# Optimization experiments

Measured on AMD Instinct MI355X. Metric: run time of the kernel, lower is better.

The kernel has to match this reference:

```python
import jax, jax.numpy as jnp
import numpy as np

N = 8192
NUM_CLASSES = 81            # background + 80 fg classes (COCO)
SCORE_THRESH = 0.05
NMS_THRESH = 0.5
NUM_DETECTIONS = 100
REG_W = (10.0, 10.0, 5.0, 5.0)
MIN_SIZE = 1.0
BBOX_XFORM_CLIP = float(np.log(1000.0 / 16.0))


def setup_inputs() -> dict:
    key = jax.random.key(0)
    k1, k2, k3, k4 = jax.random.split(key, 4)
    xy1 = jax.random.uniform(k1, (N, 2), minval=0.0, maxval=700.0)
    wh = jax.random.uniform(k2, (N, 2), minval=8.0, maxval=300.0)
    proposal = jnp.concatenate([xy1, xy1 + wh], axis=1)          # [N,4] xyxy
    class_logit = jax.random.normal(k3, (N, NUM_CLASSES), dtype=jnp.float32)
    box_regression = jax.random.normal(k4, (N, NUM_CLASSES * 4), dtype=jnp.float32) * 0.5
    return {"proposal": proposal, "class_logit": class_logit,
            "box_regression": box_regression, "image_h": 800, "image_w": 1216}


def _decode(deltas, boxes):
    # deltas [..., N, 4] (per-class), boxes [N, 4] xyxy; standard Fast R-CNN BoxCoder.decode
    wx, wy, ww, wh = REG_W
    widths = boxes[:, 2] - boxes[:, 0]
    heights = boxes[:, 3] - boxes[:, 1]
    cx = boxes[:, 0] + 0.5 * widths
    cy = boxes[:, 1] + 0.5 * heights
    dx = deltas[..., 0] / wx
    dy = deltas[..., 1] / wy
    dw = jnp.minimum(deltas[..., 2] / ww, BBOX_XFORM_CLIP)
    dh = jnp.minimum(deltas[..., 3] / wh, BBOX_XFORM_CLIP)
    pcx = dx * widths + cx
    pcy = dy * heights + cy
    pw = jnp.exp(dw) * widths
    ph = jnp.exp(dh) * heights
    return jnp.stack([pcx - 0.5 * pw, pcy - 0.5 * ph,
                      pcx + 0.5 * pw, pcy + 0.5 * ph], axis=-1)


def _iou_one(box, boxes):
    # IoU of one box [4] against all boxes [N,4]
    lt = jnp.maximum(box[:2], boxes[:, :2])
    rb = jnp.minimum(box[2:], boxes[:, 2:])
    whc = jnp.clip(rb - lt, 0.0)
    inter = whc[:, 0] * whc[:, 1]
    a1 = (box[2] - box[0]) * (box[3] - box[1])
    a2 = (boxes[:, 2] - boxes[:, 0]) * (boxes[:, 3] - boxes[:, 1])
    return inter / (a1 + a2 - inter + 1e-12)


def _nms_per_class(boxes, scores):
    # Sequential greedy NMS: pick highest score, suppress IoU>thresh, repeat.
    # boxes [N,4], scores [N] (already 0 where filtered). Returns top NUM_DETECTIONS.
    def step(scores_w, _):
        j = jnp.argmax(scores_w)
        s = scores_w[j]
        valid = s > 0.0
        bj = boxes[j]
        iou = _iou_one(bj, boxes)                         # [N]
        new = jnp.where(iou > NMS_THRESH, 0.0, scores_w).at[j].set(0.0)
        new = jnp.where(valid, new, scores_w)
        return new, (bj, s, valid)
    _, (sel_b, sel_s, sel_v) = jax.lax.scan(step, scores, None, length=NUM_DETECTIONS)
    return sel_b, sel_s, sel_v                            # [D,4], [D], [D]


def reference(proposal, class_logit, box_regression, image_h, image_w):
    pred_score = jax.nn.softmax(class_logit, axis=-1)     # [N, C]
    deltas = box_regression.reshape(N, NUM_CLASSES, 4)
    fg_deltas = jnp.transpose(deltas[:, 1:, :], (1, 0, 2))  # [C-1, N, 4]
    boxes = _decode(fg_deltas, proposal)                    # [C-1, N, 4]
    # clip to image (process_box)
    W = jnp.float32(image_w); H = jnp.float32(image_h)
    x1 = jnp.clip(boxes[..., 0], 0.0, W)
    y1 = jnp.clip(boxes[..., 1], 0.0, H)
    x2 = jnp.clip(boxes[..., 2], 0.0, W)
    y2 = jnp.clip(boxes[..., 3], 0.0, H)
    boxes = jnp.stack([x1, y1, x2, y2], axis=-1)            # [C-1, N, 4]
    keep_size = ((x2 - x1) >= MIN_SIZE) & ((y2 - y1) >= MIN_SIZE)
    scores = jnp.transpose(pred_score[:, 1:])               # [C-1, N]
    scores = jnp.where((scores >= SCORE_THRESH) & keep_size, scores, 0.0)
    sel_b, sel_s, sel_v = jax.vmap(_nms_per_class)(boxes, scores)  # [C-1,D,...]
    out_boxes = sel_b.reshape(-1, 4)                         # [(C-1)*D, 4]
    out_scores = sel_s.reshape(-1)
    out_labels = jnp.repeat(jnp.arange(1, NUM_CLASSES, dtype=jnp.int32), NUM_DETECTIONS)
    out_valid = sel_v.reshape(-1)
    return out_boxes, out_scores, out_labels, out_valid
```

## Files before the change

kernel.cpp:

```cpp
#include <hip/hip_runtime.h>
#include <hip/hip_bf16.h>

#define NN 8192
#define NC 81
#define FG 80
#define ND 100
#define SH 8
#define CAPS 128
#define CPADI 32
#define MAXK 384
#define KW6 6
#define KROW 8
#define BBOX_CLIP 4.135166556742356f

__global__ __launch_bounds__(256) void decode_kernel(
    const float* __restrict__ prop,
    const float* __restrict__ logit,
    const float* __restrict__ reg,
    const int* __restrict__ ih, const int* __restrict__ iw,
    int* __restrict__ counts,
    float* __restrict__ boxes0,
    float* __restrict__ cbox,
    float* __restrict__ cscore)
{
    const int n = blockIdx.x * 4 + (threadIdx.x >> 6);
    const int shard = blockIdx.x & (SH - 1);
    const int lane = threadIdx.x & 63;
    const float* lrow = logit + (long)n * NC;

    float v1 = lrow[lane];
    float v2 = (lane < NC - 64) ? lrow[64 + lane] : -1e30f;
    float m = fmaxf(v1, v2);
#pragma unroll
    for (int off = 32; off; off >>= 1) m = fmaxf(m, __shfl_xor(m, off));
    float e = expf(v1 - m) + ((lane < NC - 64) ? expf(v2 - m) : 0.0f);
#pragma unroll
    for (int off = 32; off; off >>= 1) e += __shfl_xor(e, off);

    const float W = (float)iw[0];
    const float H = (float)ih[0];
    const float4 p = *(const float4*)(prop + n * 4);
    const float pw = p.z - p.x, ph = p.w - p.y;
    const float pcx = p.x + 0.5f * pw, pcy = p.y + 0.5f * ph;

    for (int c = 1 + lane; c <= FG; c += 64) {
        float score = expf(lrow[c] - m) / e;
        const float4 d = *(const float4*)(reg + (long)n * (NC * 4) + c * 4);
        float dx = d.x / 10.0f;
        float dy = d.y / 10.0f;
        float dw = fminf(d.z / 5.0f, BBOX_CLIP);
        float dh = fminf(d.w / 5.0f, BBOX_CLIP);
        float ncx = dx * pw + pcx;
        float ncy = dy * ph + pcy;
        float nw = expf(dw) * pw;
        float nh = expf(dh) * ph;
        float bx1 = ncx - 0.5f * nw, by1 = ncy - 0.5f * nh;
        float bx2 = ncx + 0.5f * nw, by2 = ncy + 0.5f * nh;
        bx1 = fminf(fmaxf(bx1, 0.0f), W);
        by1 = fminf(fmaxf(by1, 0.0f), H);
        bx2 = fminf(fmaxf(bx2, 0.0f), W);
        by2 = fminf(fmaxf(by2, 0.0f), H);
        bool keep = ((bx2 - bx1) >= 1.0f) && ((by2 - by1) >= 1.0f);

        if (n == 0) {
            float* b0 = boxes0 + (c - 1) * 4;
            b0[0] = bx1; b0[1] = by1; b0[2] = bx2; b0[3] = by2;
        }
        if (score >= 0.05f && keep) {
            const int slot = (c - 1) * SH + shard;
            int pos = atomicAdd(&counts[slot * CPADI], 1);
            if (pos < CAPS) {
                float* cb = cbox + ((long)slot * CAPS + pos) * 4;
                cb[0] = bx1; cb[1] = by1; cb[2] = bx2; cb[3] = by2;
                cscore[slot * CAPS + pos] = score;
            }
        }
    }
}

__global__ __launch_bounds__(1024) void nms_kernel(
    const int* __restrict__ counts,
    const float* __restrict__ boxes0,
    const float* __restrict__ cbox,
    const float* __restrict__ cscore,
    float* __restrict__ out)
{
    __shared__ __align__(16) float  s_sc[MAXK];
    __shared__ float4 s_ubox[MAXK];
    __shared__ int    s_sidx[MAXK];
    __shared__ float4 s_box[MAXK];
    __shared__ float  s_ss[MAXK];
    __shared__ unsigned long long s_row[MAXK * KROW];

    const int c = blockIdx.x;
    const int t = threadIdx.x;
    const int lane = t & 63;
    const int wv = t >> 6;

    int cnt0 = min(counts[(c * SH + 0) * CPADI], CAPS);
    int cnt1 = min(counts[(c * SH + 1) * CPADI], CAPS);
    int cnt2 = min(counts[(c * SH + 2) * CPADI], CAPS);
    int cnt3 = min(counts[(c * SH + 3) * CPADI], CAPS);
    int cnt4 = min(counts[(c * SH + 4) * CPADI], CAPS);
    int cnt5 = min(counts[(c * SH + 5) * CPADI], CAPS);
    int cnt6 = min(counts[(c * SH + 6) * CPADI], CAPS);
    int cnt7 = min(counts[(c * SH + 7) * CPADI], CAPS);
    int K = cnt0 + cnt1 + cnt2 + cnt3 + cnt4 + cnt5 + cnt6 + cnt7;
    if (K > MAXK) K = MAXK;
    const int KW = (K + 63) >> 6;

    for (int i = t; i < MAXK * KROW; i += 1024) s_row[i] = 0ull;
    for (int i = K + t; i < MAXK; i += 1024) {
        s_sc[i] = 0.0f;
        s_ss[i] = 0.0f;
        s_box[i] = make_float4(0.f, 0.f, 0.f, 0.f);
    }
    {
        const int s = t >> 7;
        const int i = t & (CAPS - 1);
        int mycnt = cnt0;
        if (s == 1) mycnt = cnt1; if (s == 2) mycnt = cnt2;
        if (s == 3) mycnt = cnt3; if (s == 4) mycnt = cnt4;
        if (s == 5) mycnt = cnt5; if (s == 6) mycnt = cnt6;
        if (s == 7) mycnt = cnt7;
        int offs = 0;
        if (s > 0) offs += cnt0; if (s > 1) offs += cnt1;
        if (s > 2) offs += cnt2; if (s > 3) offs += cnt3;
        if (s > 4) offs += cnt4; if (s > 5) offs += cnt5;
        if (s > 6) offs += cnt6;
        if (i < mycnt) {
            int d = offs + i;
            if (d < MAXK) {
                const long src = (long)(c * SH + s) * CAPS + i;
                s_sc[d] = cscore[src];
                s_ubox[d] = *(const float4*)(cbox + src * 4);
            }
        }
    }
    __syncthreads();

    if (t < K) {
        const float si = s_sc[t];
        const float4* s4 = (const float4*)s_sc;
        const int nch = (K + 3) >> 2;
        int r = 0;
        for (int ch = 0; ch < nch; ++ch) {
            const float4 sj = s4[ch];
            const int j = ch * 4;
            r += (sj.x > si) || (sj.x == si && (j + 0) < t);
            r += (sj.y > si) || (sj.y == si && (j + 1) < t);
            r += (sj.z > si) || (sj.z == si && (j + 2) < t);
            r += (sj.w > si) || (sj.w == si && (j + 3) < t);
        }
        s_sidx[r] = t;
    }
    __syncthreads();

    if (t < K) {
        const int i = s_sidx[t];
        s_box[t] = s_ubox[i];
        s_ss[t] = s_sc[i];
    }
    __syncthreads();

    float4 colb[KW6];
    float a2c[KW6];
#pragma unroll
    for (int w = 0; w < KW6; ++w) {
        const float4 b = s_box[w * 64 + lane];
        colb[w] = b;
        a2c[w] = (b.z - b.x) * (b.w - b.y);
    }

    for (int r = wv; r < K; r += 16) {
        const float4 rb = s_box[r];
        const float a1 = (rb.z - rb.x) * (rb.w - rb.y);
        const int w0 = r >> 6;
#pragma unroll
        for (int w = 0; w < KW6; ++w) {
            if (w >= w0 && w < KW) {
                const int j = w * 64 + lane;
                const float lx = fmaxf(rb.x, colb[w].x);
                const float ly = fmaxf(rb.y, colb[w].y);
                const float rx = fminf(rb.z, colb[w].z);
                const float ry = fminf(rb.w, colb[w].w);
                const float cw = fmaxf(rx - lx, 0.0f);
                const float ch = fmaxf(ry - ly, 0.0f);
                const float inter = cw * ch;
                const float iou = inter / (a1 + a2c[w] - inter + 1e-12f);
                const bool sup = (iou > 0.5f) && (j > r);
                const unsigned long long msk = __ballot(sup);
                if (lane == 0) s_row[r * KROW + w] = msk;
            }
        }
    }
    __syncthreads();

    if (wv != 0) return;

    float* ob = out + (long)c * ND * 4;
    float* os = out + (long)FG * ND * 4 + c * ND;
    float* ol = os + FG * ND;
    float* ov = ol + FG * ND;
    const float lab = (float)(c + 1);

    unsigned long long aw0, aw1, aw2, aw3, aw4, aw5;
#define INIW(W) ((K >= (W)*64 + 64) ? ~0ull : ((K <= (W)*64) ? 0ull : ((~0ull) >> (64 - (K - (W)*64)))))
    aw0 = INIW(0); aw1 = INIW(1); aw2 = INIW(2);
    aw3 = INIW(3); aw4 = INIW(4); aw5 = INIW(5);
#undef INIW

    int kept = 0;
#define SWEEP(W, AW)                                                        \
    while (AW != 0 && kept < ND) {                                          \
        const int b_ = __builtin_ctzll(AW);                                 \
        const int i_ = (W) * 64 + b_;                                       \
        const unsigned long long* rp_ = s_row + i_ * KROW;                  \
        unsigned long long q0_ = rp_[0], q1_ = rp_[1], q2_ = rp_[2],        \
                           q3_ = rp_[3], q4_ = rp_[4], q5_ = rp_[5];        \
        if (lane == 0) {                                                    \
            const float4 kb = s_box[i_];                                    \
            ob[kept * 4 + 0] = kb.x; ob[kept * 4 + 1] = kb.y;               \
            ob[kept * 4 + 2] = kb.z; ob[kept * 4 + 3] = kb.w;               \
            os[kept] = s_ss[i_]; ol[kept] = lab; ov[kept] = 1.0f;           \
        }                                                                   \
        kept++;                                                             \
        aw0 &= ~q0_; aw1 &= ~q1_; aw2 &= ~q2_;                              \
        aw3 &= ~q3_; aw4 &= ~q4_; aw5 &= ~q5_;                              \
        AW &= ~(1ull << b_);   \
    }
    SWEEP(0, aw0) SWEEP(1, aw1) SWEEP(2, aw2)
    SWEEP(3, aw3) SWEEP(4, aw4) SWEEP(5, aw5)
#undef SWEEP

    const float b0x1 = boxes0[c * 4 + 0], b0y1 = boxes0[c * 4 + 1];
    const float b0x2 = boxes0[c * 4 + 2], b0y2 = boxes0[c * 4 + 3];
    for (int d = kept + lane; d < ND; d += 64) {
        ob[d * 4 + 0] = b0x1; ob[d * 4 + 1] = b0y1;
        ob[d * 4 + 2] = b0x2; ob[d * 4 + 3] = b0y2;
        os[d] = 0.0f; ol[d] = lab; ov[d] = 0.0f;
    }
}

extern "C" void kernel_launch(void* const* d_in, const int* in_sizes, int n_in,
                              void* d_out, int out_size, void* d_ws, size_t ws_size,
                              hipStream_t stream) {
    const float* prop  = (const float*)d_in[0];
    const float* logit = (const float*)d_in[1];
    const float* reg   = (const float*)d_in[2];
    const int*   ih    = (const int*)d_in[3];
    const int*   iw    = (const int*)d_in[4];
    float* out = (float*)d_out;

    char* ws = (char*)d_ws;
    int*   counts = (int*)ws;
    float* boxes0 = (float*)(ws + 81920);
    float* cscore = (float*)(ws + 90112);
    float* cbox   = (float*)(ws + 90112 + (size_t)FG * SH * CAPS * 4);

    hipMemsetAsync(counts, 0, FG * SH * CPADI * sizeof(int), stream);
    decode_kernel<<<NN / 4, 256, 0, stream>>>(prop, logit, reg, ih, iw,
                                              counts, boxes0, cbox, cscore);
    nms_kernel<<<FG, 1024, 0, stream>>>(counts, boxes0, cbox, cscore, out);
}
```

Measured before the change: 116.2 us.

## Replace serial greedy NMS sweep with wave-parallel fixed-point iteration

The serial per-kept-box ctz sweep is replaced by a wave-parallel fixed-point iteration. Each lane computes whether its box is suppressed by any earlier still-kept box, and all lanes update together through ballots until the keep masks stop changing. Kept boxes are then scattered to the output in parallel using popcount rank selection, with float4 stores. The full IoU mask is now computed without the upper-triangle restriction and the zero-init of the row matrix is removed, relying on the lower-triangle mask (ltm) instead. KROW is padded to 9 to avoid LDS bank conflicts on lane-strided row reads. The iteration count depends on the suppression chain depth and can be large in the worst case.

New measurement: 106.7 us. 8.2% less time.

```diff
diff --git a/kernel.cpp b/kernel.cpp
--- a/kernel.cpp
+++ b/kernel.cpp
@@ -10,7 +10,7 @@
 #define CPADI 32
 #define MAXK 384
 #define KW6 6
-#define KROW 8
+#define KROW 9
 #define BBOX_CLIP 4.135166556742356f
 
 __global__ __launch_bounds__(256) void decode_kernel(
@@ -109,7 +109,7 @@
     if (K > MAXK) K = MAXK;
     const int KW = (K + 63) >> 6;
 
-    for (int i = t; i < MAXK * KROW; i += 1024) s_row[i] = 0ull;
+
     for (int i = K + t; i < MAXK; i += 1024) {
         s_sc[i] = 0.0f;
         s_ss[i] = 0.0f;
@@ -175,11 +175,9 @@
     for (int r = wv; r < K; r += 16) {
         const float4 rb = s_box[r];
         const float a1 = (rb.z - rb.x) * (rb.w - rb.y);
-        const int w0 = r >> 6;
 #pragma unroll
         for (int w = 0; w < KW6; ++w) {
-            if (w >= w0 && w < KW) {
-                const int j = w * 64 + lane;
+            if (w < KW) {
                 const float lx = fmaxf(rb.x, colb[w].x);
                 const float ly = fmaxf(rb.y, colb[w].y);
                 const float rx = fminf(rb.z, colb[w].z);
@@ -188,8 +186,7 @@
                 const float ch = fmaxf(ry - ly, 0.0f);
                 const float inter = cw * ch;
                 const float iou = inter / (a1 + a2c[w] - inter + 1e-12f);
-                const bool sup = (iou > 0.5f) && (j > r);
-                const unsigned long long msk = __ballot(sup);
+                const unsigned long long msk = __ballot(iou > 0.5f);
                 if (lane == 0) s_row[r * KROW + w] = msk;
             }
         }
@@ -197,6 +194,57 @@
     __syncthreads();
 
     if (wv != 0) return;
+
+#define INIW(W) ((K >= (W)*64 + 64) ? ~0ull : ((K <= (W)*64) ? 0ull : ((~0ull) >> (64 - (K - (W)*64)))))
+    const unsigned long long va0 = INIW(0), va1 = INIW(1), va2 = INIW(2);
+    const unsigned long long va3 = INIW(3), va4 = INIW(4), va5 = INIW(5);
+#undef INIW
+
+    const unsigned long long ltm = (1ull << lane) - 1ull;
+
+    unsigned long long v0 = va0, v1 = va1, v2 = va2;
+    unsigned long long v3 = va3, v4 = va4, v5 = va5;
+
+    for (int it = 0; it < MAXK; ++it) {
+        unsigned long long nv0, nv1, nv2, nv3, nv4, nv5;
+        {
+            const unsigned long long* rp = s_row + (unsigned)(0 * 64 + lane) * KROW;
+            unsigned long long s = rp[0] & v0 & ltm;
+            nv0 = __ballot(s == 0ull) & va0;
+        }
+        {
+            const unsigned long long* rp = s_row + (unsigned)(1 * 64 + lane) * KROW;
+            unsigned long long s = (rp[0] & v0) | (rp[1] & v1 & ltm);
+            nv1 = __ballot(s == 0ull) & va1;
+        }
+        {
+            const unsigned long long* rp = s_row + (unsigned)(2 * 64 + lane) * KROW;
+            unsigned long long s = (rp[0] & v0) | (rp[1] & v1) | (rp[2] & v2 & ltm);
+            nv2 = __ballot(s == 0ull) & va2;
+        }
+        {
+            const unsigned long long* rp = s_row + (unsigned)(3 * 64 + lane) * KROW;
+            unsigned long long s = (rp[0] & v0) | (rp[1] & v1) | (rp[2] & v2) |
+                                   (rp[3] & v3 & ltm);
+            nv3 = __ballot(s == 0ull) & va3;
+        }
+        {
+            const unsigned long long* rp = s_row + (unsigned)(4 * 64 + lane) * KROW;
+            unsigned long long s = (rp[0] & v0) | (rp[1] & v1) | (rp[2] & v2) |
+                                   (rp[3] & v3) | (rp[4] & v4 & ltm);
+            nv4 = __ballot(s == 0ull) & va4;
+        }
+        {
+            const unsigned long long* rp = s_row + (unsigned)(5 * 64 + lane) * KROW;
+            unsigned long long s = (rp[0] & v0) | (rp[1] & v1) | (rp[2] & v2) |
+                                   (rp[3] & v3) | (rp[4] & v4) | (rp[5] & v5 & ltm);
+            nv5 = __ballot(s == 0ull) & va5;
+        }
+        const unsigned long long diff = (nv0 ^ v0) | (nv1 ^ v1) | (nv2 ^ v2) |
+                                        (nv3 ^ v3) | (nv4 ^ v4) | (nv5 ^ v5);
+        v0 = nv0; v1 = nv1; v2 = nv2; v3 = nv3; v4 = nv4; v5 = nv5;
+        if (diff == 0ull) break;
+    }
 
     float* ob = out + (long)c * ND * 4;
     float* os = out + (long)FG * ND * 4 + c * ND;
@@ -204,41 +252,42 @@
     float* ov = ol + FG * ND;
     const float lab = (float)(c + 1);
 
-    unsigned long long aw0, aw1, aw2, aw3, aw4, aw5;
-#define INIW(W) ((K >= (W)*64 + 64) ? ~0ull : ((K <= (W)*64) ? 0ull : ((~0ull) >> (64 - (K - (W)*64)))))
-    aw0 = INIW(0); aw1 = INIW(1); aw2 = INIW(2);
-    aw3 = INIW(3); aw4 = INIW(4); aw5 = INIW(5);
-#undef INIW
-
-    int kept = 0;
-#define SWEEP(W, AW)                                                        \
-    while (AW != 0 && kept < ND) {                                          \
-        const int b_ = __builtin_ctzll(AW);                                 \
-        const int i_ = (W) * 64 + b_;                                       \
-        const unsigned long long* rp_ = s_row + i_ * KROW;                  \
-        unsigned long long q0_ = rp_[0], q1_ = rp_[1], q2_ = rp_[2],        \
-                           q3_ = rp_[3], q4_ = rp_[4], q5_ = rp_[5];        \
-        if (lane == 0) {                                                    \
-            const float4 kb = s_box[i_];                                    \
-            ob[kept * 4 + 0] = kb.x; ob[kept * 4 + 1] = kb.y;               \
-            ob[kept * 4 + 2] = kb.z; ob[kept * 4 + 3] = kb.w;               \
-            os[kept] = s_ss[i_]; ol[kept] = lab; ov[kept] = 1.0f;           \
-        }                                                                   \
-        kept++;                                                             \
-        aw0 &= ~q0_; aw1 &= ~q1_; aw2 &= ~q2_;                              \
-        aw3 &= ~q3_; aw4 &= ~q4_; aw5 &= ~q5_;                              \
-        AW &= ~(1ull << b_);   \
-    }
-    SWEEP(0, aw0) SWEEP(1, aw1) SWEEP(2, aw2)
-    SWEEP(3, aw3) SWEEP(4, aw4) SWEEP(5, aw5)
-#undef SWEEP
+    const int p0 = __popcll(v0), p1 = __popcll(v1), p2 = __popcll(v2);
+    const int p3 = __popcll(v3), p4 = __popcll(v4);
+    const int total = p0 + p1 + p2 + p3 + p4 + __popcll(v5);
+    const int kept = total < ND ? total : ND;
 
     const float b0x1 = boxes0[c * 4 + 0], b0y1 = boxes0[c * 4 + 1];
     const float b0x2 = boxes0[c * 4 + 2], b0y2 = boxes0[c * 4 + 3];
-    for (int d = kept + lane; d < ND; d += 64) {
-        ob[d * 4 + 0] = b0x1; ob[d * 4 + 1] = b0y1;
-        ob[d * 4 + 2] = b0x2; ob[d * 4 + 3] = b0y2;
-        os[d] = 0.0f; ol[d] = lab; ov[d] = 0.0f;
+
+    for (int d = lane; d < ND; d += 64) {
+        if (d < kept) {
+            int rr = d;
+            unsigned long long x;
+            int wbase;
+            if (rr < p0) { x = v0; wbase = 0; }
+            else { rr -= p0;
+                if (rr < p1) { x = v1; wbase = 64; }
+                else { rr -= p1;
+                    if (rr < p2) { x = v2; wbase = 128; }
+                    else { rr -= p2;
+                        if (rr < p3) { x = v3; wbase = 192; }
+                        else { rr -= p3;
+                            if (rr < p4) { x = v4; wbase = 256; }
+                            else { rr -= p4; x = v5; wbase = 320; }
+                        }
+                    }
+                }
+            }
+            for (int k = 0; k < rr; ++k) x &= x - 1ull;
+            const int i_d = wbase + __builtin_ctzll(x);
+            const float4 kb = s_box[i_d];
+            *(float4*)(ob + d * 4) = kb;
+            os[d] = s_ss[i_d]; ol[d] = lab; ov[d] = 1.0f;
+        } else {
+            *(float4*)(ob + d * 4) = make_float4(b0x1, b0y1, b0x2, b0y2);
+            os[d] = 0.0f; ol[d] = lab; ov[d] = 0.0f;
+        }
     }
 }
 
```
